# Kernel optimization log

Measured on AMD Instinct MI355X. Metric: run time of the kernel, lower is better.

## Reference

```python
import jax, jax.numpy as jnp
import numpy as np
from math import factorial, sqrt

# (mul, l) lists after e3nn normalization/mul-splitting (muls already aligned)
RS1 = [(256, 0), (256, 1), (256, 2)]
RS2 = [(256, 1), (256, 1), (256, 2)]


def _su2_cg(j1, m1, j2, m2, j3, m3):
    # Racah formula for SU(2) Clebsch-Gordan <j1 m1 j2 m2 | j3 m3> (e3nn convention)
    if m3 != m1 + m2:
        return 0.0
    vmin = max(-j1 + j2 + m3, -j1 + m1, 0)
    vmax = min(j2 + j3 + m1, j3 - j1 + j2, j3 + m3)
    f = factorial
    C = sqrt((2 * j3 + 1)
             * f(j3 + j1 - j2) * f(j3 - j1 + j2) * f(j1 + j2 - j3) * f(j3 + m3) * f(j3 - m3)
             / (f(j1 + j2 + j3 + 1) * f(j1 - m1) * f(j1 + m1) * f(j2 - m2) * f(j2 + m2)))
    S = 0.0
    for v in range(vmin, vmax + 1):
        S += (-1.0) ** (v + j2 + m2) * (f(j2 + j3 + m1 - v) * f(j1 - m1 + v)
             / (f(v) * f(j3 - j1 + j2 - v) * f(j3 + m3 - v) * f(v + j1 - j2 - m3)))
    return C * S


def _su2_cg_tensor(j1, j2, j3):
    mat = np.zeros((2 * j1 + 1, 2 * j2 + 1, 2 * j3 + 1))
    for m1 in range(-j1, j1 + 1):
        for m2 in range(-j2, j2 + 1):
            m3 = m1 + m2
            if abs(m3) <= j3:
                mat[j1 + m1, j2 + m2, j3 + m3] = _su2_cg(j1, m1, j2, m2, j3, m3)
    return mat / sqrt(2 * j3 + 1)  # Wigner-3j normalization


def _q(l):
    # change of basis real -> complex spherical harmonics (e3nn convention)
    q = np.zeros((2 * l + 1, 2 * l + 1), dtype=np.complex128)
    for m in range(-l, 0):
        q[l + m, l + abs(m)] = 1.0 / sqrt(2)
        q[l + m, l - abs(m)] = -1j / sqrt(2)
    q[l, l] = 1.0
    for m in range(1, l + 1):
        q[l + m, l + abs(m)] = (-1) ** m / sqrt(2)
        q[l + m, l - abs(m)] = 1j * (-1) ** m / sqrt(2)
    return (-1j) ** l * q


def _wigner3j(l1, l2, l3):
    # real-basis Wigner 3j tensor, shape (2l1+1, 2l2+1, 2l3+1)
    C = _su2_cg_tensor(l1, l2, l3)
    Q1, Q2, Q3 = _q(l1), _q(l2), _q(l3)
    C = np.einsum('ij,kl,nm,ikn->jlm', Q1, Q2, np.conj(Q3), C)
    assert np.abs(C.imag).max() < 1e-6
    return C.real


# precomputed CG blocks C[(l, l1, l2)] of shape (2l+1, 2l1+1, 2l2+1), scaled by sqrt(2l+1)
CG = {}
for (_mul1, _l1), (_mul2, _l2) in zip(RS1, RS2):
    if _l1 != 0 and _l2 != 0:
        for _l in range(abs(_l1 - _l2), _l1 + _l2 + 1):
            CG[(_l, _l1, _l2)] = jnp.asarray(_wigner3j(_l, _l1, _l2) * sqrt(2 * _l + 1), dtype=jnp.float32)


def _forward(features_1, features_2):
    size = features_1.shape[:-1]
    f1 = features_1.reshape(-1, features_1.shape[-1])
    f2 = features_2.reshape(-1, features_2.shape[-1])
    B = f1.shape[0]
    out, i1, i2 = [], 0, 0
    for (mul, l1), (_, l2) in zip(RS1, RS2):
        d1, d2 = 2 * l1 + 1, 2 * l2 + 1
        x1 = f1[:, i1:i1 + mul * d1].reshape(B, mul, d1)
        i1 += mul * d1
        x2 = f2[:, i2:i2 + mul * d2].reshape(B, mul, d2)
        i2 += mul * d2
        if l1 == 0 or l2 == 0:
            # CG with a scalar is (a multiple of) identity -> elementwise product
            out.append((x1 * x2).reshape(B, -1))
        else:
            for l in range(abs(l1 - l2), l1 + l2 + 1):
                C = CG[(l, l1, l2)]  # (2l+1, d1, d2)
                out.append(jnp.einsum('ijk,bmj,bmk->bmi', C, x1, x2).reshape(B, -1))
    return jnp.concatenate(out, axis=1).reshape(*size, -1)


def setup_inputs() -> dict:
    key = jax.random.key(0)
    k1, k2 = jax.random.split(key)
    n1 = sum(m * (2 * l + 1) for m, l in RS1)  # 2304
    n2 = sum(m * (2 * l + 1) for m, l in RS2)  # 2816
    B = 8192
    return {
        'features_1': jax.random.normal(k1, (B, n1), dtype=jnp.float32),
        'features_2': jax.random.normal(k2, (B, n2), dtype=jnp.float32),
    }


def reference(features_1, features_2):
    return _forward(features_1, features_2)
```

## Files before the change

### kernel.cpp

```cpp
#include <hip/hip_runtime.h>

namespace cg {

constexpr double fact(int n) {
  double r = 1.0;
  for (int i = 2; i <= n; ++i) r *= (double)i;
  return r;
}

constexpr double csqrt(double x) {
  if (x <= 0.0) return 0.0;
  double g = x < 1.0 ? 1.0 : x;
  for (int i = 0; i < 80; ++i) g = 0.5 * (g + x / g);
  return g;
}

struct cplx { double re, im; };
constexpr cplx cmul(cplx a, cplx b) {
  return cplx{a.re * b.re - a.im * b.im, a.re * b.im + a.im * b.re};
}

constexpr double su2_cg(int j1, int m1, int j2, int m2, int j3, int m3) {
  if (m3 != m1 + m2) return 0.0;
  int vmin = -j1 + j2 + m3;
  if (-j1 + m1 > vmin) vmin = -j1 + m1;
  if (0 > vmin) vmin = 0;
  int vmax = j2 + j3 + m1;
  if (j3 - j1 + j2 < vmax) vmax = j3 - j1 + j2;
  if (j3 + m3 < vmax) vmax = j3 + m3;
  const double C = csqrt((2.0 * j3 + 1.0)
      * fact(j3 + j1 - j2) * fact(j3 - j1 + j2) * fact(j1 + j2 - j3)
      * fact(j3 + m3) * fact(j3 - m3)
      / (fact(j1 + j2 + j3 + 1) * fact(j1 - m1) * fact(j1 + m1)
         * fact(j2 - m2) * fact(j2 + m2)));
  double S = 0.0;
  for (int v = vmin; v <= vmax; ++v) {
    const double sgn = ((v + j2 + m2) & 1) ? -1.0 : 1.0;
    S += sgn * (fact(j2 + j3 + m1 - v) * fact(j1 - m1 + v)
         / (fact(v) * fact(j3 - j1 + j2 - v) * fact(j3 + m3 - v)
            * fact(v + j1 - j2 - m3)));
  }
  return C * S;
}

template <int L> struct QMat { cplx q[2 * L + 1][2 * L + 1]; };

template <int L>
constexpr QMat<L> make_q() {
  QMat<L> Q{};
  const double s = 1.0 / csqrt(2.0);
  for (int m = -L; m < 0; ++m) {
    Q.q[L + m][L - m] = cplx{s, 0.0};
    Q.q[L + m][L + m] = cplx{0.0, -s};
  }
  Q.q[L][L] = cplx{1.0, 0.0};
  for (int m = 1; m <= L; ++m) {
    const double sg = (m & 1) ? -1.0 : 1.0;
    Q.q[L + m][L + m] = cplx{sg * s, 0.0};
    Q.q[L + m][L - m] = cplx{0.0, sg * s};
  }
  cplx p{1.0, 0.0};
  for (int t = 0; t < L; ++t) p = cmul(p, cplx{0.0, -1.0});
  for (int r = 0; r < 2 * L + 1; ++r)
    for (int c = 0; c < 2 * L + 1; ++c)
      Q.q[r][c] = cmul(p, Q.q[r][c]);
  return Q;
}

template <int L, int L1, int L2>
struct W3 { float t[2 * L + 1][2 * L1 + 1][2 * L2 + 1]; };

template <int L, int L1, int L2>
constexpr W3<L, L1, L2> wigner() {
  const QMat<L>  Q1 = make_q<L>();
  const QMat<L1> Q2 = make_q<L1>();
  const QMat<L2> Q3 = make_q<L2>();
  double C[2 * L + 1][2 * L1 + 1][2 * L2 + 1] = {};
  for (int m1 = -L; m1 <= L; ++m1)
    for (int m2 = -L1; m2 <= L1; ++m2) {
      const int m3 = m1 + m2;
      if (m3 >= -L2 && m3 <= L2)
        C[L + m1][L1 + m2][L2 + m3] = su2_cg(L, m1, L1, m2, L2, m3);
    }
  const double scale = csqrt(2.0 * L + 1.0) / csqrt(2.0 * L2 + 1.0);
  W3<L, L1, L2> R{};
  for (int j = 0; j < 2 * L + 1; ++j)
    for (int l = 0; l < 2 * L1 + 1; ++l)
      for (int m = 0; m < 2 * L2 + 1; ++m) {
        cplx acc{0.0, 0.0};
        for (int i = 0; i < 2 * L + 1; ++i) {
          const cplx q1 = Q1.q[i][j];
          if (q1.re == 0.0 && q1.im == 0.0) continue;
          for (int k = 0; k < 2 * L1 + 1; ++k) {
            const cplx q2 = Q2.q[k][l];
            if (q2.re == 0.0 && q2.im == 0.0) continue;
            const cplx q12 = cmul(q1, q2);
            for (int n = 0; n < 2 * L2 + 1; ++n) {
              const double c = C[i][k][n];
              if (c == 0.0) continue;
              const cplx q3c{Q3.q[n][m].re, -Q3.q[n][m].im};
              const cplx term = cmul(q12, q3c);
              acc.re += term.re * c;
              acc.im += term.im * c;
            }
          }
        }
        R.t[j][l][m] = (float)(acc.re * scale);
      }
  return R;
}

constexpr W3<0, 1, 1> W011 = wigner<0, 1, 1>();
constexpr W3<1, 1, 1> W111 = wigner<1, 1, 1>();
constexpr W3<2, 1, 1> W211 = wigner<2, 1, 1>();
constexpr W3<0, 2, 2> W022 = wigner<0, 2, 2>();
constexpr W3<1, 2, 2> W122 = wigner<1, 2, 2>();
constexpr W3<2, 2, 2> W222 = wigner<2, 2, 2>();
constexpr W3<3, 2, 2> W322 = wigner<3, 2, 2>();
constexpr W3<4, 2, 2> W422 = wigner<4, 2, 2>();

}


template <int L, int L1, int L2>
__device__ __forceinline__ void contract(const cg::W3<L, L1, L2>& W,
                                         const float (&p)[2 * L1 + 1][2 * L2 + 1],
                                         float* __restrict__ o) {
#pragma unroll
  for (int i = 0; i < 2 * L + 1; ++i) {
    float acc = 0.0f;
#pragma unroll
    for (int j = 0; j < 2 * L1 + 1; ++j)
#pragma unroll
      for (int k = 0; k < 2 * L2 + 1; ++k) {
        const float c = W.t[i][j][k];
        if (c != 0.0f) acc = __builtin_fmaf(c, p[j][k], acc);
      }
    o[i] = acc;
  }
}

__global__ __launch_bounds__(256) void tp_kernel(
    const float* __restrict__ f1, const float* __restrict__ f2,
    float* __restrict__ out, int B) {
  __shared__ __align__(16) float lds[9472];
  const int b = blockIdx.x;
  if (b >= B) return;
  const int t = threadIdx.x;

  {
    const float4* s1 = reinterpret_cast<const float4*>(f1 + (size_t)b * 2304);
    const float4* s2 = reinterpret_cast<const float4*>(f2 + (size_t)b * 2816);
    float4* l4 = reinterpret_cast<float4*>(lds);
#pragma unroll
    for (int k = 0; k < 2; ++k) l4[t + k * 256] = s1[t + k * 256];
    if (t < 64) l4[512 + t] = s1[512 + t];
#pragma unroll
    for (int k = 0; k < 2; ++k) l4[576 + t + k * 256] = s2[t + k * 256];
    if (t < 192) l4[1088 + t] = s2[512 + t];
  }
  __syncthreads();

  const int m = t;
  float r0[3];
  float o0, o1[3], o2[5];
  float q0, q1[3], q2[5], q3[7], q4[9];
  {
    const float s = lds[m];
#pragma unroll
    for (int k = 0; k < 3; ++k) r0[k] = s * lds[2304 + m * 3 + k];
  }
  {
    float a[3], c[3];
#pragma unroll
    for (int j = 0; j < 3; ++j) a[j] = lds[256 + m * 3 + j];
#pragma unroll
    for (int k = 0; k < 3; ++k) c[k] = lds[2304 + 768 + m * 3 + k];
    float p[3][3];
#pragma unroll
    for (int j = 0; j < 3; ++j)
#pragma unroll
      for (int k = 0; k < 3; ++k) p[j][k] = a[j] * c[k];
    contract<0, 1, 1>(cg::W011, p, &o0);
    contract<1, 1, 1>(cg::W111, p, o1);
    contract<2, 1, 1>(cg::W211, p, o2);
  }
  {
    float a[5], c[5];
#pragma unroll
    for (int j = 0; j < 5; ++j) a[j] = lds[1024 + m * 5 + j];
#pragma unroll
    for (int k = 0; k < 5; ++k) c[k] = lds[2304 + 1536 + m * 5 + k];
    float p[5][5];
#pragma unroll
    for (int j = 0; j < 5; ++j)
#pragma unroll
      for (int k = 0; k < 5; ++k) p[j][k] = a[j] * c[k];
    contract<0, 2, 2>(cg::W022, p, &q0);
    contract<1, 2, 2>(cg::W122, p, q1);
    contract<2, 2, 2>(cg::W222, p, q2);
    contract<3, 2, 2>(cg::W322, p, q3);
    contract<4, 2, 2>(cg::W422, p, q4);
  }
  __syncthreads();

#pragma unroll
  for (int k = 0; k < 3; ++k) lds[m * 3 + k] = r0[k];
  lds[768 + m] = o0;
#pragma unroll
  for (int i = 0; i < 3; ++i) lds[1024 + m * 3 + i] = o1[i];
#pragma unroll
  for (int i = 0; i < 5; ++i) lds[1792 + m * 5 + i] = o2[i];
  lds[3072 + m] = q0;
#pragma unroll
  for (int i = 0; i < 3; ++i) lds[3328 + m * 3 + i] = q1[i];
#pragma unroll
  for (int i = 0; i < 5; ++i) lds[4096 + m * 5 + i] = q2[i];
#pragma unroll
  for (int i = 0; i < 7; ++i) lds[5376 + m * 7 + i] = q3[i];
#pragma unroll
  for (int i = 0; i < 9; ++i) lds[7168 + m * 9 + i] = q4[i];
  __syncthreads();

  {
    const float4* l4 = reinterpret_cast<const float4*>(lds);
    float4* dst = reinterpret_cast<float4*>(out + (size_t)b * 9472);
#pragma unroll
    for (int k = 0; k < 9; ++k) dst[t + k * 256] = l4[t + k * 256];
    if (t < 64) dst[2304 + t] = l4[2304 + t];
  }
}

extern "C" void kernel_launch(void* const* d_in, const int* in_sizes, int n_in,
                              void* d_out, int out_size, void* d_ws, size_t ws_size,
                              hipStream_t stream) {
  const float* f1 = (const float*)d_in[0];
  const float* f2 = (const float*)d_in[1];
  float* out = (float*)d_out;
  const int B = in_sizes[0] / 2304;
  tp_kernel<<<B, 256, 0, stream>>>(f1, f2, out, B);
}
```

Measured before the change: 94.67 us.

## Split each batch row across four 64-thread single-wave blocks

Instead of one 256-thread block per batch row, the kernel launches four 64-thread (one-wavefront) blocks per row, each handling a quarter of the multiplicity channels. Each block stages only its slice of inputs and outputs in a much smaller shared buffer (about 9.5 KB instead of 37 KB). The aim is higher occupancy and cheaper block-level barriers, since each barrier now covers a single wave. In exchange there are four times as many blocks, and the global loads and stores are smaller, more fragmented and partly predicated.

```diff
diff --git a/kernel.cpp b/kernel.cpp
--- a/kernel.cpp
+++ b/kernel.cpp
@@ -140,62 +140,66 @@
   }
 }
 
-__global__ __launch_bounds__(256) void tp_kernel(
+__global__ __launch_bounds__(64) void tp_kernel(
     const float* __restrict__ f1, const float* __restrict__ f2,
     float* __restrict__ out, int B) {
-  __shared__ __align__(16) float lds[9472];
-  const int b = blockIdx.x;
+  __shared__ __align__(16) float Wr[2368];
+  const int bid = blockIdx.x;
+  const int b = bid >> 2;
   if (b >= B) return;
-  const int t = threadIdx.x;
+  const int w = bid & 3;
+  const int l = threadIdx.x;
 
   {
     const float4* s1 = reinterpret_cast<const float4*>(f1 + (size_t)b * 2304);
     const float4* s2 = reinterpret_cast<const float4*>(f2 + (size_t)b * 2816);
-    float4* l4 = reinterpret_cast<float4*>(lds);
-#pragma unroll
-    for (int k = 0; k < 2; ++k) l4[t + k * 256] = s1[t + k * 256];
-    if (t < 64) l4[512 + t] = s1[512 + t];
-#pragma unroll
-    for (int k = 0; k < 2; ++k) l4[576 + t + k * 256] = s2[t + k * 256];
-    if (t < 192) l4[1088 + t] = s2[512 + t];
+    float4* L4 = reinterpret_cast<float4*>(Wr);
+    if (l < 16) L4[l] = s1[16 * w + l];
+    if (l < 48) L4[16 + l] = s1[64 + 48 * w + l];
+    L4[64 + l] = s1[256 + 80 * w + l];
+    if (l < 16) L4[128 + l] = s1[256 + 80 * w + 64 + l];
+    if (l < 48) L4[144 + l] = s2[48 * w + l];
+    if (l < 48) L4[192 + l] = s2[192 + 48 * w + l];
+    L4[240 + l] = s2[384 + 80 * w + l];
+    if (l < 16) L4[304 + l] = s2[384 + 80 * w + 64 + l];
   }
   __syncthreads();
 
-  const int m = t;
+  const float s0 = Wr[l];
+  float ca[3], a1[3], cb[3], a2[5], cc[5];
+#pragma unroll
+  for (int k = 0; k < 3; ++k) ca[k] = Wr[576 + l * 3 + k];
+#pragma unroll
+  for (int j = 0; j < 3; ++j) a1[j] = Wr[64 + l * 3 + j];
+#pragma unroll
+  for (int k = 0; k < 3; ++k) cb[k] = Wr[768 + l * 3 + k];
+#pragma unroll
+  for (int j = 0; j < 5; ++j) a2[j] = Wr[256 + l * 5 + j];
+#pragma unroll
+  for (int k = 0; k < 5; ++k) cc[k] = Wr[960 + l * 5 + k];
+
   float r0[3];
+#pragma unroll
+  for (int k = 0; k < 3; ++k) r0[k] = s0 * ca[k];
+
   float o0, o1[3], o2[5];
-  float q0, q1[3], q2[5], q3[7], q4[9];
-  {
-    const float s = lds[m];
-#pragma unroll
-    for (int k = 0; k < 3; ++k) r0[k] = s * lds[2304 + m * 3 + k];
-  }
-  {
-    float a[3], c[3];
-#pragma unroll
-    for (int j = 0; j < 3; ++j) a[j] = lds[256 + m * 3 + j];
-#pragma unroll
-    for (int k = 0; k < 3; ++k) c[k] = lds[2304 + 768 + m * 3 + k];
+  {
     float p[3][3];
 #pragma unroll
     for (int j = 0; j < 3; ++j)
 #pragma unroll
-      for (int k = 0; k < 3; ++k) p[j][k] = a[j] * c[k];
+      for (int k = 0; k < 3; ++k) p[j][k] = a1[j] * cb[k];
     contract<0, 1, 1>(cg::W011, p, &o0);
     contract<1, 1, 1>(cg::W111, p, o1);
     contract<2, 1, 1>(cg::W211, p, o2);
   }
-  {
-    float a[5], c[5];
-#pragma unroll
-    for (int j = 0; j < 5; ++j) a[j] = lds[1024 + m * 5 + j];
-#pragma unroll
-    for (int k = 0; k < 5; ++k) c[k] = lds[2304 + 1536 + m * 5 + k];
+  float q0, q1[3], q2[5], q3[7], q4[9];
+  {
     float p[5][5];
 #pragma unroll
     for (int j = 0; j < 5; ++j)
 #pragma unroll
-      for (int k = 0; k < 5; ++k) p[j][k] = a[j] * c[k];
+      for (int k = 0; k < 5; ++k) p[j][k] = a2[j] * cc[k];
     contract<0, 2, 2>(cg::W022, p, &q0);
     contract<1, 2, 2>(cg::W122, p, q1);
     contract<2, 2, 2>(cg::W222, p, q2);
@@ -205,29 +209,40 @@
   __syncthreads();
 
 #pragma unroll
-  for (int k = 0; k < 3; ++k) lds[m * 3 + k] = r0[k];
-  lds[768 + m] = o0;
-#pragma unroll
-  for (int i = 0; i < 3; ++i) lds[1024 + m * 3 + i] = o1[i];
-#pragma unroll
-  for (int i = 0; i < 5; ++i) lds[1792 + m * 5 + i] = o2[i];
-  lds[3072 + m] = q0;
-#pragma unroll
-  for (int i = 0; i < 3; ++i) lds[3328 + m * 3 + i] = q1[i];
-#pragma unroll
-  for (int i = 0; i < 5; ++i) lds[4096 + m * 5 + i] = q2[i];
-#pragma unroll
-  for (int i = 0; i < 7; ++i) lds[5376 + m * 7 + i] = q3[i];
-#pragma unroll
-  for (int i = 0; i < 9; ++i) lds[7168 + m * 9 + i] = q4[i];
+  for (int k = 0; k < 3; ++k) Wr[l * 3 + k] = r0[k];
+  Wr[192 + l] = o0;
+#pragma unroll
+  for (int i = 0; i < 3; ++i) Wr[256 + l * 3 + i] = o1[i];
+#pragma unroll
+  for (int i = 0; i < 5; ++i) Wr[448 + l * 5 + i] = o2[i];
+  Wr[768 + l] = q0;
+#pragma unroll
+  for (int i = 0; i < 3; ++i) Wr[832 + l * 3 + i] = q1[i];
+#pragma unroll
+  for (int i = 0; i < 5; ++i) Wr[1024 + l * 5 + i] = q2[i];
+#pragma unroll
+  for (int i = 0; i < 7; ++i) Wr[1344 + l * 7 + i] = q3[i];
+#pragma unroll
+  for (int i = 0; i < 9; ++i) Wr[1792 + l * 9 + i] = q4[i];
   __syncthreads();
 
   {
-    const float4* l4 = reinterpret_cast<const float4*>(lds);
-    float4* dst = reinterpret_cast<float4*>(out + (size_t)b * 9472);
-#pragma unroll
-    for (int k = 0; k < 9; ++k) dst[t + k * 256] = l4[t + k * 256];
-    if (t < 64) dst[2304 + t] = l4[2304 + t];
+    const float4* OF = reinterpret_cast<const float4*>(Wr);
+    float4* D = reinterpret_cast<float4*>(out + (size_t)b * 9472);
+    if (l < 48) D[48 * w + l] = OF[l];
+    if (l < 16) D[192 + 16 * w + l] = OF[48 + l];
+    if (l < 48) D[256 + 48 * w + l] = OF[64 + l];
+    D[448 + 80 * w + l] = OF[112 + l];
+    if (l < 16) D[448 + 80 * w + 64 + l] = OF[176 + l];
+    if (l < 16) D[768 + 16 * w + l] = OF[192 + l];
+    if (l < 48) D[832 + 48 * w + l] = OF[208 + l];
+    D[1024 + 80 * w + l] = OF[256 + l];
+    if (l < 16) D[1024 + 80 * w + 64 + l] = OF[320 + l];
+    D[1344 + 112 * w + l] = OF[336 + l];
+    if (l < 48) D[1344 + 112 * w + 64 + l] = OF[400 + l];
+    D[1792 + 144 * w + l] = OF[448 + l];
+    D[1792 + 144 * w + 64 + l] = OF[512 + l];
+    if (l < 16) D[1792 + 144 * w + 128 + l] = OF[576 + l];
   }
 }
 
@@ -238,5 +253,5 @@
   const float* f2 = (const float*)d_in[1];
   float* out = (float*)d_out;
   const int B = in_sizes[0] / 2304;
-  tp_kernel<<<B, 256, 0, stream>>>(f1, f2, out, B);
-}
+  tp_kernel<<<B * 4, 64, 0, stream>>>(f1, f2, out, B);
+}
```

Result: slower. 96.90 us (+2.4%).
